# Kernel tuning notes

Measured on AMD Instinct MI355X. Metric: run time of the kernel, lower is better.

The kernel has to match this reference:

```python
import jax, jax.numpy as jnp
import numpy as np


def _lstm_layer(x, W, U, b):
    """Keras-style LSTM (gate order i,f,c,o). x: (B,T,F). Returns (hs: (B,T,H), h_last: (B,H))."""
    B, T, F = x.shape
    H = U.shape[0]
    # Precompute input projections for all timesteps: (T, B, 4H)
    zx = jnp.einsum('btf,fk->tbk', x, W) + b

    def step(carry, zx_t):
        h, c = carry
        z = zx_t + h @ U  # (B, 4H)
        i, f, g, o = jnp.split(z, 4, axis=-1)
        i = jax.nn.sigmoid(i)
        f = jax.nn.sigmoid(f)
        g = jnp.tanh(g)
        o = jax.nn.sigmoid(o)
        c = f * c + i * g
        h = o * jnp.tanh(c)
        return (h, c), h

    h0 = jnp.zeros((B, H), dtype=x.dtype)
    c0 = jnp.zeros((B, H), dtype=x.dtype)
    (h_last, _), hs = jax.lax.scan(step, (h0, c0), zx)
    return jnp.transpose(hs, (1, 0, 2)), h_last


def setup_inputs() -> dict:
    key = jax.random.key(0)
    ks = jax.random.split(key, 8)
    B, T, F, H, L = 512, 128, 64, 1024, 1
    s = 0.05
    return {
        'x': jax.random.normal(ks[0], (B, T, F), dtype=jnp.float32),
        'W1': jax.random.normal(ks[1], (F, 4 * H), dtype=jnp.float32) * s,
        'U1': jax.random.normal(ks[2], (H, 4 * H), dtype=jnp.float32) * s,
        'b1': jnp.zeros((4 * H,), dtype=jnp.float32),
        'W2': jax.random.normal(ks[3], (H, 4 * H), dtype=jnp.float32) * s,
        'U2': jax.random.normal(ks[4], (H, 4 * H), dtype=jnp.float32) * s,
        'b2': jnp.zeros((4 * H,), dtype=jnp.float32),
        'Wd': jax.random.normal(ks[5], (H, L), dtype=jnp.float32) * s,
        'bd': jnp.zeros((L,), dtype=jnp.float32),
    }


def reference(x, W1, U1, b1, W2, U2, b2, Wd, bd):
    # Layer 1: return_sequences=True (dropout inactive at inference)
    h1_seq, _ = _lstm_layer(x, W1, U1, b1)
    # Layer 2: return_sequences=False -> last hidden state
    _, h2_last = _lstm_layer(h1_seq, W2, U2, b2)
    # Dense sigmoid head
    return jax.nn.sigmoid(h2_last @ Wd + bd)
```

## Files before the change

### kernel.cpp

```cpp
#include <hip/hip_runtime.h>
#include <hip/hip_bf16.h>
#include <cstdint>


typedef __attribute__((ext_vector_type(8))) _Float16 half8;
typedef __attribute__((ext_vector_type(4))) float    float4v;

__device__ __forceinline__ float sigf(float x) { return 1.0f / (1.0f + __expf(-x)); }
__device__ __forceinline__ float tanhfast(float x) { return 2.0f * sigf(2.0f * x) - 1.0f; }

static constexpr size_t HPS = 32ull * 32 * 512;

struct FragSet {
    half8 A[4][4];
    half8 B[4][4];
};

__global__ __launch_bounds__(256, 1) void fused_step(
    int s,
    const _Float16* __restrict__ xp,
    const _Float16* __restrict__ P1,
    const _Float16* __restrict__ P2,
    const float* __restrict__ b1, float* __restrict__ c1, _Float16* __restrict__ h1p,
    const float* __restrict__ b2, float* __restrict__ c2, _Float16* __restrict__ h2p)
{
    const int b    = blockIdx.x;
    const int role = (b >> 3) & 1;
    const int tile = ((b >> 4) << 3) | (b & 7);

    const _Float16 *As0, *As1, *Pk;
    const float* bias; float* cs; _Float16* hop;
    int KC0, KCB, KCT;
    if (role == 0) {
        const int t = s; if (t >= 128) return;
        As0 = xp + (size_t)t * 32768;  KC0 = 2;
        As1 = h1p + (size_t)(t & 1) * HPS;
        Pk = P1; KCB = 34; KCT = 34;
        bias = b1; cs = c1;
        hop = h1p + (size_t)(1 - (t & 1)) * HPS;
    } else {
        const int t = s - 1; if (t < 0) return;
        As0 = h1p + (size_t)(1 - (t & 1)) * HPS; KC0 = 32;
        As1 = h2p + (size_t)(t & 1) * HPS;
        Pk = P2; KCB = 64; KCT = 64;
        bias = b2; cs = c2;
        hop = h2p + (size_t)(1 - (t & 1)) * HPS;
    }

    const int tid = threadIdx.x;
    const int w   = tid >> 6;
    const int l   = tid & 63;
    const int q   = l >> 4;
    const int c16 = l & 15;
    const int mh  = w & 1;
    const int nh  = w >> 1;

    const int m0  = (tile >> 5) * 128;
    const int n0  = (tile & 31) * 32;
    const int mG0 = (m0 >> 4) + mh * 4;

    const size_t l8 = (size_t)l * 8;

    const _Float16* bp[4];
#pragma unroll
    for (int g = 0; g < 4; ++g)
        bp[g] = Pk + ((size_t)(g * 64 + (n0 >> 4) + nh) * KCB) * 512 + l8;

    float4v acc[4][4] = {};

    auto loadS = [&](int st, FragSet& S) {
#pragma unroll
        for (int kcl = 0; kcl < 4; ++kcl) {
            const int kc = st * 4 + kcl;
            const _Float16* ab; size_t astr;
            if (kc < KC0) { ab = As0 + (size_t)kc * 512;         astr = (size_t)KC0 * 512; }
            else          { ab = As1 + (size_t)(kc - KC0) * 512; astr = 32ull * 512; }
            ab += (size_t)mG0 * astr + l8;
#pragma unroll
            for (int ms = 0; ms < 4; ++ms)
                S.A[ms][kcl] = *(const half8*)(ab + (size_t)ms * astr);
#pragma unroll
            for (int g = 0; g < 4; ++g)
                S.B[kcl][g] = *(const half8*)(bp[g] + (size_t)kc * 512);
        }
    };
    auto computeS = [&](const FragSet& S) {
#pragma unroll
        for (int kcl = 0; kcl < 4; ++kcl)
#pragma unroll
            for (int g = 0; g < 4; ++g)
#pragma unroll
                for (int ms = 0; ms < 4; ++ms)
                    acc[g][ms] = __builtin_amdgcn_mfma_f32_16x16x32_f16(
                        S.A[ms][kcl], S.B[kcl][g], acc[g][ms], 0, 0, 0);
    };

    const int NS = KCT >> 2;
    FragSet S0, S1;
    loadS(0, S0);
    for (int st = 0; st + 2 <= NS; st += 2) {
        loadS(st + 1, S1);
        computeS(S0);
        if (st + 2 < NS) loadS(st + 2, S0);
        computeS(S1);
    }
    if (KCT & 3) {
        half8 At[4][2], Bt[2][4];
#pragma unroll
        for (int kcl = 0; kcl < 2; ++kcl) {
            const int kc = NS * 4 + kcl;
            const _Float16* ab = As1 + (size_t)(kc - KC0) * 512
                               + (size_t)mG0 * (32ull * 512) + l8;
#pragma unroll
            for (int ms = 0; ms < 4; ++ms)
                At[ms][kcl] = *(const half8*)(ab + (size_t)ms * (32ull * 512));
#pragma unroll
            for (int g = 0; g < 4; ++g)
                Bt[kcl][g] = *(const half8*)(bp[g] + (size_t)kc * 512);
        }
#pragma unroll
        for (int kcl = 0; kcl < 2; ++kcl)
#pragma unroll
            for (int g = 0; g < 4; ++g)
#pragma unroll
                for (int ms = 0; ms < 4; ++ms)
                    acc[g][ms] = __builtin_amdgcn_mfma_f32_16x16x32_f16(
                        At[ms][kcl], Bt[kcl][g], acc[g][ms], 0, 0, 0);
    }

    const int ng = n0 + nh * 16 + c16;
    const float bi  = bias[ng];
    const float bff = bias[1024 + ng];
    const float bg  = bias[2048 + ng];
    const float bo  = bias[3072 + ng];
    const int kcH   = n0 >> 5;
    const int laneW = (nh * 2 + (c16 >> 3)) << 4;
    const int jW    = c16 & 7;
#pragma unroll
    for (int ms = 0; ms < 4; ++ms) {
        const int mG = mG0 + ms;
        _Float16* hg = hop + ((size_t)(mG * 32 + kcH)) * 512 + (size_t)laneW * 8 + jW;
#pragma unroll
        for (int i = 0; i < 4; ++i) {
            const int m = m0 + mh * 64 + ms * 16 + q * 4 + i;
            const float zi = acc[0][ms][i] + bi;
            const float zf = acc[1][ms][i] + bff;
            const float zg = acc[2][ms][i] + bg;
            const float zo = acc[3][ms][i] + bo;
            const float ig = sigf(zi);
            const float fg = sigf(zf);
            const float gg = tanhfast(zg);
            const float og = sigf(zo);
            const size_t cidx = (size_t)m * 1024 + ng;
            const float cc = fg * cs[cidx] + ig * gg;
            cs[cidx] = cc;
            hg[(q * 4 + i) * 8] = (_Float16)(og * tanhfast(cc));
        }
    }
}

__global__ void pack_weights(const float* __restrict__ W, const float* __restrict__ U,
                             int KA, int KC, _Float16* __restrict__ out)
{
    const size_t e = (size_t)blockIdx.x * blockDim.x + threadIdx.x;
    const size_t total = (size_t)256 * KC * 512;
    if (e >= total) return;
    const int j    = (int)(e & 7);
    const int lane = (int)((e >> 3) & 63);
    const size_t g = e >> 9;
    const int kc  = (int)(g % KC);
    const int ntG = (int)(g / KC);
    const int col = ntG * 16 + (lane & 15);
    const int k   = kc * 32 + (lane >> 4) * 8 + j;
    const float v = (k < KA) ? W[(size_t)k * 4096 + col]
                             : U[(size_t)(k - KA) * 4096 + col];
    out[e] = (_Float16)v;
}

__global__ void pack_x(const float* __restrict__ x, _Float16* __restrict__ xp)
{
    const int e = blockIdx.x * blockDim.x + threadIdx.x;
    if (e >= 512 * 128 * 64) return;
    const int j  = e & 7;
    const int l  = (e >> 3) & 63;
    const int g  = e >> 9;
    const int kc = g & 1;
    const int tm = g >> 1;
    const int mG = tm & 31;
    const int t  = tm >> 5;
    const int m  = mG * 16 + (l & 15);
    const int f  = kc * 32 + (l >> 4) * 8 + j;
    xp[e] = (_Float16)x[((size_t)m * 128 + t) * 64 + f];
}

__global__ __launch_bounds__(64) void dense_head(const _Float16* __restrict__ h2p,
                                                 const float* __restrict__ Wd,
                                                 const float* __restrict__ bd,
                                                 float* __restrict__ out)
{
    const int mG = blockIdx.x;
    const int l  = threadIdx.x;
    float s = 0.0f;
    for (int kc = 0; kc < 32; ++kc) {
        half8 f = *(const half8*)(h2p + ((size_t)(mG * 32 + kc)) * 512 + (size_t)l * 8);
        const int kb = kc * 32 + (l >> 4) * 8;
#pragma unroll
        for (int j = 0; j < 8; ++j) s += (float)f[j] * Wd[kb + j];
    }
    s += __shfl_xor(s, 16);
    s += __shfl_xor(s, 32);
    if (l < 16) out[mG * 16 + l] = 1.0f / (1.0f + __expf(-(s + bd[0])));
}


extern "C" void kernel_launch(void* const* d_in, const int* in_sizes, int n_in,
                              void* d_out, int out_size, void* d_ws, size_t ws_size,
                              hipStream_t stream)
{
    const float* x  = (const float*)d_in[0];
    const float* W1 = (const float*)d_in[1];
    const float* U1 = (const float*)d_in[2];
    const float* b1 = (const float*)d_in[3];
    const float* W2 = (const float*)d_in[4];
    const float* U2 = (const float*)d_in[5];
    const float* b2 = (const float*)d_in[6];
    const float* Wd = (const float*)d_in[7];
    const float* bd = (const float*)d_in[8];
    float* out = (float*)d_out;

    char* ws = (char*)d_ws;
    size_t off = 0;
    auto alloc = [&](size_t bytes) {
        char* p = ws + off;
        off = (off + bytes + 255) & ~(size_t)255;
        return p;
    };
    _Float16* xp  = (_Float16*)alloc(512ull * 128 * 64 * 2);
    _Float16* P1  = (_Float16*)alloc(256ull * 34 * 512 * 2);
    _Float16* P2  = (_Float16*)alloc(256ull * 64 * 512 * 2);
    _Float16* h1p = (_Float16*)alloc(2ull * HPS * 2);
    _Float16* h2p = (_Float16*)alloc(2ull * HPS * 2);
    float*    c1  = (float*)alloc(512ull * 1024 * 4);
    float*    c2  = (float*)alloc(512ull * 1024 * 4);

    hipMemsetAsync(c1, 0, 512ull * 1024 * 4, stream);
    hipMemsetAsync(c2, 0, 512ull * 1024 * 4, stream);
    hipMemsetAsync(h1p, 0, HPS * 2, stream);
    hipMemsetAsync(h2p, 0, HPS * 2, stream);

    pack_x<<<(512 * 128 * 64 + 255) / 256, 256, 0, stream>>>(x, xp);
    pack_weights<<<(256 * 34 * 512 + 255) / 256, 256, 0, stream>>>(W1, U1, 64, 34, P1);
    pack_weights<<<(256 * 64 * 512 + 255) / 256, 256, 0, stream>>>(W2, U2, 1024, 64, P2);

    for (int s = 0; s <= 128; ++s) {
        fused_step<<<256, 256, 0, stream>>>(s, xp, P1, P2,
                                            b1, c1, h1p, b2, c2, h2p);
    }
    dense_head<<<32, 64, 0, stream>>>(h2p, Wd, bd, out);
}
```

Measured before the change: 3.482 ms.

## Fuse per-timestep launches into one persistent kernel with grid barrier

```diff
diff --git a/kernel.cpp b/kernel.cpp
--- a/kernel.cpp
+++ b/kernel.cpp
@@ -16,36 +16,39 @@
     half8 B[4][4];
 };
 
-__global__ __launch_bounds__(256, 1) void fused_step(
-    int s,
+__device__ __forceinline__ void grid_barrier(int* cnt, int* gen, int nb)
+{
+    __syncthreads();
+    if (threadIdx.x == 0) {
+        __builtin_amdgcn_fence(__ATOMIC_RELEASE, "agent");
+        const int g = __hip_atomic_load(gen, __ATOMIC_RELAXED, __HIP_MEMORY_SCOPE_AGENT);
+        const int a = __hip_atomic_fetch_add(cnt, 1, __ATOMIC_ACQ_REL, __HIP_MEMORY_SCOPE_AGENT);
+        if (a == nb - 1) {
+            __hip_atomic_store(cnt, 0, __ATOMIC_RELAXED, __HIP_MEMORY_SCOPE_AGENT);
+            __hip_atomic_fetch_add(gen, 1, __ATOMIC_RELEASE, __HIP_MEMORY_SCOPE_AGENT);
+        } else {
+            while (__hip_atomic_load(gen, __ATOMIC_RELAXED, __HIP_MEMORY_SCOPE_AGENT) == g)
+                __builtin_amdgcn_s_sleep(1);
+        }
+        __builtin_amdgcn_fence(__ATOMIC_ACQUIRE, "agent");
+    }
+    __syncthreads();
+}
+
+__global__ __launch_bounds__(256, 1) void fused_all(
     const _Float16* __restrict__ xp,
     const _Float16* __restrict__ P1,
     const _Float16* __restrict__ P2,
     const float* __restrict__ b1, float* __restrict__ c1, _Float16* __restrict__ h1p,
-    const float* __restrict__ b2, float* __restrict__ c2, _Float16* __restrict__ h2p)
-{
+    const float* __restrict__ b2, float* __restrict__ c2, _Float16* __restrict__ h2p,
+    int* __restrict__ bar)
+{
+    int* cnt = bar;
+    int* gen = bar + 64;
+
     const int b    = blockIdx.x;
     const int role = (b >> 3) & 1;
     const int tile = ((b >> 4) << 3) | (b & 7);
-
-    const _Float16 *As0, *As1, *Pk;
-    const float* bias; float* cs; _Float16* hop;
-    int KC0, KCB, KCT;
-    if (role == 0) {
-        const int t = s; if (t >= 128) return;
-        As0 = xp + (size_t)t * 32768;  KC0 = 2;
-        As1 = h1p + (size_t)(t & 1) * HPS;
-        Pk = P1; KCB = 34; KCT = 34;
-        bias = b1; cs = c1;
-        hop = h1p + (size_t)(1 - (t & 1)) * HPS;
-    } else {
-        const int t = s - 1; if (t < 0) return;
-        As0 = h1p + (size_t)(1 - (t & 1)) * HPS; KC0 = 32;
-        As1 = h2p + (size_t)(t & 1) * HPS;
-        Pk = P2; KCB = 64; KCT = 64;
-        bias = b2; cs = c2;
-        hop = h2p + (size_t)(1 - (t & 1)) * HPS;
-    }
 
     const int tid = threadIdx.x;
     const int w   = tid >> 6;
@@ -58,75 +61,18 @@
     const int m0  = (tile >> 5) * 128;
     const int n0  = (tile & 31) * 32;
     const int mG0 = (m0 >> 4) + mh * 4;
-
     const size_t l8 = (size_t)l * 8;
+
+    const _Float16* Pk = role ? P2 : P1;
+    const int KCB = role ? 64 : 34;
+    const int KC0 = role ? 32 : 2;
+    const float* bias = role ? b2 : b1;
+    float* cs = role ? c2 : c1;
 
     const _Float16* bp[4];
 #pragma unroll
     for (int g = 0; g < 4; ++g)
         bp[g] = Pk + ((size_t)(g * 64 + (n0 >> 4) + nh) * KCB) * 512 + l8;
-
-    float4v acc[4][4] = {};
-
-    auto loadS = [&](int st, FragSet& S) {
-#pragma unroll
-        for (int kcl = 0; kcl < 4; ++kcl) {
-            const int kc = st * 4 + kcl;
-            const _Float16* ab; size_t astr;
-            if (kc < KC0) { ab = As0 + (size_t)kc * 512;         astr = (size_t)KC0 * 512; }
-            else          { ab = As1 + (size_t)(kc - KC0) * 512; astr = 32ull * 512; }
-            ab += (size_t)mG0 * astr + l8;
-#pragma unroll
-            for (int ms = 0; ms < 4; ++ms)
-                S.A[ms][kcl] = *(const half8*)(ab + (size_t)ms * astr);
-#pragma unroll
-            for (int g = 0; g < 4; ++g)
-                S.B[kcl][g] = *(const half8*)(bp[g] + (size_t)kc * 512);
-        }
-    };
-    auto computeS = [&](const FragSet& S) {
-#pragma unroll
-        for (int kcl = 0; kcl < 4; ++kcl)
-#pragma unroll
-            for (int g = 0; g < 4; ++g)
-#pragma unroll
-                for (int ms = 0; ms < 4; ++ms)
-                    acc[g][ms] = __builtin_amdgcn_mfma_f32_16x16x32_f16(
-                        S.A[ms][kcl], S.B[kcl][g], acc[g][ms], 0, 0, 0);
-    };
-
-    const int NS = KCT >> 2;
-    FragSet S0, S1;
-    loadS(0, S0);
-    for (int st = 0; st + 2 <= NS; st += 2) {
-        loadS(st + 1, S1);
-        computeS(S0);
-        if (st + 2 < NS) loadS(st + 2, S0);
-        computeS(S1);
-    }
-    if (KCT & 3) {
-        half8 At[4][2], Bt[2][4];
-#pragma unroll
-        for (int kcl = 0; kcl < 2; ++kcl) {
-            const int kc = NS * 4 + kcl;
-            const _Float16* ab = As1 + (size_t)(kc - KC0) * 512
-                               + (size_t)mG0 * (32ull * 512) + l8;
-#pragma unroll
-            for (int ms = 0; ms < 4; ++ms)
-                At[ms][kcl] = *(const half8*)(ab + (size_t)ms * (32ull * 512));
-#pragma unroll
-            for (int g = 0; g < 4; ++g)
-                Bt[kcl][g] = *(const half8*)(bp[g] + (size_t)kc * 512);
-        }
-#pragma unroll
-        for (int kcl = 0; kcl < 2; ++kcl)
-#pragma unroll
-            for (int g = 0; g < 4; ++g)
-#pragma unroll
-                for (int ms = 0; ms < 4; ++ms)
-                    acc[g][ms] = __builtin_amdgcn_mfma_f32_16x16x32_f16(
-                        At[ms][kcl], Bt[kcl][g], acc[g][ms], 0, 0, 0);
-    }
 
     const int ng = n0 + nh * 16 + c16;
     const float bi  = bias[ng];
@@ -136,26 +82,108 @@
     const int kcH   = n0 >> 5;
     const int laneW = (nh * 2 + (c16 >> 3)) << 4;
     const int jW    = c16 & 7;
-#pragma unroll
-    for (int ms = 0; ms < 4; ++ms) {
-        const int mG = mG0 + ms;
-        _Float16* hg = hop + ((size_t)(mG * 32 + kcH)) * 512 + (size_t)laneW * 8 + jW;
-#pragma unroll
-        for (int i = 0; i < 4; ++i) {
-            const int m = m0 + mh * 64 + ms * 16 + q * 4 + i;
-            const float zi = acc[0][ms][i] + bi;
-            const float zf = acc[1][ms][i] + bff;
-            const float zg = acc[2][ms][i] + bg;
-            const float zo = acc[3][ms][i] + bo;
-            const float ig = sigf(zi);
-            const float fg = sigf(zf);
-            const float gg = tanhfast(zg);
-            const float og = sigf(zo);
-            const size_t cidx = (size_t)m * 1024 + ng;
-            const float cc = fg * cs[cidx] + ig * gg;
-            cs[cidx] = cc;
-            hg[(q * 4 + i) * 8] = (_Float16)(og * tanhfast(cc));
+    const int NS    = KCB >> 2;
+
+    for (int s = 0; s <= 128; ++s) {
+        const int t = role ? s - 1 : s;
+        if (t >= 0 && t < 128) {
+            const int par = t & 1;
+            const _Float16 *As0, *As1; _Float16* hop;
+            if (role == 0) {
+                As0 = xp + (size_t)t * 32768;
+                As1 = h1p + (size_t)par * HPS;
+                hop = h1p + (size_t)(1 - par) * HPS;
+            } else {
+                As0 = h1p + (size_t)(1 - par) * HPS;
+                As1 = h2p + (size_t)par * HPS;
+                hop = h2p + (size_t)(1 - par) * HPS;
+            }
+
+            float4v acc[4][4] = {};
+
+            auto loadS = [&](int st, FragSet& S) {
+#pragma unroll
+                for (int kcl = 0; kcl < 4; ++kcl) {
+                    const int kc = st * 4 + kcl;
+                    const _Float16* ab; size_t astr;
+                    if (kc < KC0) { ab = As0 + (size_t)kc * 512;         astr = (size_t)KC0 * 512; }
+                    else          { ab = As1 + (size_t)(kc - KC0) * 512; astr = 32ull * 512; }
+                    ab += (size_t)mG0 * astr + l8;
+#pragma unroll
+                    for (int ms = 0; ms < 4; ++ms)
+                        S.A[ms][kcl] = *(const half8*)(ab + (size_t)ms * astr);
+#pragma unroll
+                    for (int g = 0; g < 4; ++g)
+                        S.B[kcl][g] = *(const half8*)(bp[g] + (size_t)kc * 512);
+                }
+            };
+            auto computeS = [&](const FragSet& S) {
+#pragma unroll
+                for (int kcl = 0; kcl < 4; ++kcl)
+#pragma unroll
+                    for (int g = 0; g < 4; ++g)
+#pragma unroll
+                        for (int ms = 0; ms < 4; ++ms)
+                            acc[g][ms] = __builtin_amdgcn_mfma_f32_16x16x32_f16(
+                                S.A[ms][kcl], S.B[kcl][g], acc[g][ms], 0, 0, 0);
+            };
+
+            FragSet S0, S1;
+            loadS(0, S0);
+            for (int st = 0; st + 2 <= NS; st += 2) {
+                loadS(st + 1, S1);
+                computeS(S0);
+                if (st + 2 < NS) loadS(st + 2, S0);
+                computeS(S1);
+            }
+            if (KCB & 3) {
+                half8 At[4][2], Bt[2][4];
+#pragma unroll
+                for (int kcl = 0; kcl < 2; ++kcl) {
+                    const int kc = NS * 4 + kcl;
+                    const _Float16* ab = As1 + (size_t)(kc - KC0) * 512
+                                       + (size_t)mG0 * (32ull * 512) + l8;
+#pragma unroll
+                    for (int ms = 0; ms < 4; ++ms)
+                        At[ms][kcl] = *(const half8*)(ab + (size_t)ms * (32ull * 512));
+#pragma unroll
+                    for (int g = 0; g < 4; ++g)
+                        Bt[kcl][g] = *(const half8*)(bp[g] + (size_t)kc * 512);
+                }
+#pragma unroll
+                for (int kcl = 0; kcl < 2; ++kcl)
+#pragma unroll
+                    for (int g = 0; g < 4; ++g)
+#pragma unroll
+                        for (int ms = 0; ms < 4; ++ms)
+                            acc[g][ms] = __builtin_amdgcn_mfma_f32_16x16x32_f16(
+                                At[ms][kcl], Bt[kcl][g], acc[g][ms], 0, 0, 0);
+            }
+
+#pragma unroll
+            for (int ms = 0; ms < 4; ++ms) {
+                const int mG = mG0 + ms;
+                _Float16* hg = hop + ((size_t)(mG * 32 + kcH)) * 512
+                             + (size_t)laneW * 8 + jW;
+#pragma unroll
+                for (int i = 0; i < 4; ++i) {
+                    const int m = m0 + mh * 64 + ms * 16 + q * 4 + i;
+                    const float zi = acc[0][ms][i] + bi;
+                    const float zf = acc[1][ms][i] + bff;
+                    const float zg = acc[2][ms][i] + bg;
+                    const float zo = acc[3][ms][i] + bo;
+                    const float ig = sigf(zi);
+                    const float fg = sigf(zf);
+                    const float gg = tanhfast(zg);
+                    const float og = sigf(zo);
+                    const size_t cidx = (size_t)m * 1024 + ng;
+                    const float cc = fg * cs[cidx] + ig * gg;
+                    cs[cidx] = cc;
+                    hg[(q * 4 + i) * 8] = (_Float16)(og * tanhfast(cc));
+                }
+            }
         }
+        if (s < 128) grid_barrier(cnt, gen, 256);
     }
 }
 
@@ -242,19 +270,20 @@
     _Float16* h2p = (_Float16*)alloc(2ull * HPS * 2);
     float*    c1  = (float*)alloc(512ull * 1024 * 4);
     float*    c2  = (float*)alloc(512ull * 1024 * 4);
+    int*      bar = (int*)alloc(512);
 
     hipMemsetAsync(c1, 0, 512ull * 1024 * 4, stream);
     hipMemsetAsync(c2, 0, 512ull * 1024 * 4, stream);
     hipMemsetAsync(h1p, 0, HPS * 2, stream);
     hipMemsetAsync(h2p, 0, HPS * 2, stream);
+    hipMemsetAsync(bar, 0, 512, stream);
 
     pack_x<<<(512 * 128 * 64 + 255) / 256, 256, 0, stream>>>(x, xp);
     pack_weights<<<(256 * 34 * 512 + 255) / 256, 256, 0, stream>>>(W1, U1, 64, 34, P1);
     pack_weights<<<(256 * 64 * 512 + 255) / 256, 256, 0, stream>>>(W2, U2, 1024, 64, P2);
 
-    for (int s = 0; s <= 128; ++s) {
-        fused_step<<<256, 256, 0, stream>>>(s, xp, P1, P2,
-                                            b1, c1, h1p, b2, c2, h2p);
-    }
+    fused_all<<<256, 256, 0, stream>>>(xp, P1, P2,
+                                       b1, c1, h1p, b2, c2, h2p, bar);
+
     dense_head<<<32, 64, 0, stream>>>(h2p, Wd, bd, out);
 }
```

Result: slower. 4.596 ms (+32.0%).
